# Kernel optimization log

Measured on AMD Instinct MI355X. Metric: run time of the kernel, lower is better.

Reference implementation:

```python
import jax, jax.numpy as jnp
import numpy as np

UP = 8  # nn.Upsample(scale_factor=8), nearest


def _affine_grid(theta, H, W):
    # torch F.affine_grid, align_corners=False: pixel-center normalized coords
    xs = (jnp.arange(W, dtype=jnp.float32) + 0.5) * (2.0 / W) - 1.0
    ys = (jnp.arange(H, dtype=jnp.float32) + 0.5) * (2.0 / H) - 1.0
    base = jnp.stack([
        jnp.broadcast_to(xs[None, :], (H, W)),
        jnp.broadcast_to(ys[:, None], (H, W)),
        jnp.ones((H, W), jnp.float32),
    ], axis=-1)  # [H,W,3] = (x, y, 1)
    return jnp.einsum('hwk,bjk->bhwj', base, theta)  # [B,H,W,2], last dim = (x, y)


def _grid_sample(img, grid):
    # bilinear, padding_mode='zeros', align_corners=False (torch defaults)
    B, C, H, W = img.shape
    ix = ((grid[..., 0] + 1.0) * W - 1.0) * 0.5  # [B,Ho,Wo]
    iy = ((grid[..., 1] + 1.0) * H - 1.0) * 0.5
    ix0 = jnp.floor(ix)
    iy0 = jnp.floor(iy)
    wx1 = ix - ix0
    wy1 = iy - iy0

    def corner(xc, yc, w):
        valid = (xc >= 0) & (xc <= W - 1) & (yc >= 0) & (yc <= H - 1)
        xk = jnp.clip(xc, 0, W - 1).astype(jnp.int32)
        yk = jnp.clip(yc, 0, H - 1).astype(jnp.int32)
        g = jax.vmap(lambda im, yy, xx: im[:, yy, xx])(img, yk, xk)  # [B,C,Ho,Wo]
        return g * (w * valid.astype(img.dtype))[:, None, :, :]

    return (corner(ix0, iy0, (1.0 - wx1) * (1.0 - wy1))
            + corner(ix0 + 1.0, iy0, wx1 * (1.0 - wy1))
            + corner(ix0, iy0 + 1.0, (1.0 - wx1) * wy1)
            + corner(ix0 + 1.0, iy0 + 1.0, wx1 * wy1))


def setup_inputs() -> dict:
    key = jax.random.key(0)
    k1, k2 = jax.random.split(key)
    gt = jax.random.normal(k1, (8, 1, 128, 256), dtype=jnp.float32)
    theta = jax.random.normal(k2, (8, 6), dtype=jnp.float32)
    return {"gt": gt, "theta": theta, "output_sizex": 2048, "output_sizey": 1024}


def reference(gt, theta, output_sizex, output_sizey):
    onlyy = jnp.array([0., 0., 0., 0., 1., 1.], jnp.float32)
    offset = jnp.array([1., 0., 0., 0., 0., 0.], jnp.float32)
    thetay = (theta * onlyy + offset).reshape(-1, 2, 3)  # [[1,0,0],[0,t4,t5]]
    th = theta.reshape(-1, 2, 3)
    # nearest upsample x8
    gt_up = jnp.repeat(jnp.repeat(gt, UP, axis=2), UP, axis=3)
    grid = _affine_grid(th, output_sizey, output_sizex)
    box = _grid_sample(gt_up, grid)
    gridy = _affine_grid(thetay, output_sizey, output_sizex)
    boxy = _grid_sample(gt_up, gridy)
    return (box, boxy)
```

## Files before the change

kernel.cpp:

```cpp
#include <hip/hip_runtime.h>
#include <stdint.h>


typedef float vfloat4 __attribute__((ext_vector_type(4)));

constexpr int BATCH = 8;
constexpr int HI = 128, WI = 256;
constexpr int HO = 1024, WO = 2048;
constexpr size_t NPIX = (size_t)BATCH * HO * WO;

constexpr int QH = HI + 2;
constexpr int QW = WI + 2;
constexpr size_t QIMG = (size_t)QH * QW;

__global__ __launch_bounds__(256) void pad4_kernel(
    const float* __restrict__ gt, vfloat4* __restrict__ Q)
{
    const int i = blockIdx.x * 256 + threadIdx.x;
    if (i >= (int)(BATCH * QIMG)) return;
    const int b = i / (int)QIMG;
    const int r = i - b * (int)QIMG;
    const int y = r / QW - 1;
    const int x = r - (r / QW) * QW - 1;
    const float* __restrict__ g = gt + (size_t)b * (HI * WI);
    auto val = [&](int yy, int xx) -> float {
        return (yy >= 0 && yy < HI && xx >= 0 && xx < WI)
                   ? g[yy * WI + xx] : 0.0f;
    };
    vfloat4 q = { val(y, x), val(y, x + 1), val(y + 1, x), val(y + 1, x + 1) };
    Q[i] = q;
}

__global__ __launch_bounds__(256) void stn_kernel(
    const float* __restrict__ gt,
    const float* __restrict__ theta,
    const vfloat4* __restrict__ Q,
    float* __restrict__ out)
{
    const int row = blockIdx.x;
    const int b = row >> 10;
    const int h = row & (HO - 1);
    const int t = threadIdx.x;

    const float* tb = theta + b * 6;
    const float t0 = tb[0], t1 = tb[1], t2 = tb[2];
    const float t3 = tb[3], t4 = tb[4], t5 = tb[5];
    const float* __restrict__ gtb = gt + b * (HI * WI);
    const vfloat4* __restrict__ Qb = Q + (size_t)b * QIMG + QW + 1;

    const float ys = (h + 0.5f) * (2.0f / (float)HO) - 1.0f;
    const float dix = t0;
    const float diy = 0.5f * t3;

    const float gy2 = t4 * ys + t5;
    const float iyy = ((gy2 + 1.0f) * (float)HO - 1.0f) * 0.5f;
    const float fyy = floorf(iyy);
    const float wyy = iyy - fyy;
    const float vy0 = (fyy >= 0.0f && fyy <= (float)(HO - 1)) ? 1.0f : 0.0f;
    const float vy1 = (fyy >= -1.0f && fyy <= (float)(HO - 2)) ? 1.0f : 0.0f;
    const int y0 = ((int)fminf(fmaxf(fyy,        0.0f), (float)(HO - 1))) >> 3;
    const int y1 = ((int)fminf(fmaxf(fyy + 1.0f, 0.0f), (float)(HO - 1))) >> 3;
    const float wA = (1.0f - wyy) * vy0;
    const float wB = wyy * vy1;

    float* const outrow  = out + (size_t)row * WO;
    float* const outrowy = out + NPIX + (size_t)row * WO;

#pragma unroll
    for (int s = 0; s < 2; ++s) {
        const int w0s = (s << 10) + (t << 2);

        {
            const int cell = w0s >> 3;
            const float s0 = gtb[y0 * WI + cell];
            const float s1 = gtb[y1 * WI + cell];
            const float byv = s0 * wA + s1 * wB;
            const vfloat4 vb = {byv, byv, byv, byv};
            *reinterpret_cast<vfloat4*>(outrowy + w0s) = vb;
        }

        const float xn0 = (w0s + 0.5f) * (2.0f / (float)WO) - 1.0f;
        const float gx0 = t0 * xn0 + (t1 * ys + t2);
        const float gy0 = t3 * xn0 + (t4 * ys + t5);
        const float ix0 = ((gx0 + 1.0f) * (float)WO - 1.0f) * 0.5f;
        const float iy0 = ((gy0 + 1.0f) * (float)HO - 1.0f) * 0.5f;

        const float ixe = ix0 + 3.0f * dix;
        const float iye = iy0 + 3.0f * diy;
        const float ixmin = fminf(ix0, ixe), ixmax = fmaxf(ix0, ixe);
        const float iymin = fminf(iy0, iye), iymax = fmaxf(iy0, iye);
        const bool segzero = (ixmax < -1.0f) || (ixmin >= (float)WO) ||
                             (iymax < -1.0f) || (iymin >= (float)HO);
        const bool segsafe = (ixmin >= -1.0f) && (ixmax < (float)WO) &&
                             (iymin >= -1.0f) && (iymax < (float)HO);

        float px[4];
        if (segzero) {
#pragma unroll
            for (int p = 0; p < 4; ++p) px[p] = 0.0f;
        } else if (segsafe) {
            vfloat4 q[4];
            float wx[4], wy[4];
            bool cxe[4], cye[4];
#pragma unroll
            for (int p = 0; p < 4; ++p) {
                const float ixp = fmaf((float)p, dix, ix0);
                const float iyp = fmaf((float)p, diy, iy0);
                const float fx = floorf(ixp), fy = floorf(iyp);
                wx[p] = ixp - fx;  wy[p] = iyp - fy;
                const int xi = (int)fx, yi = (int)fy;
                const int cx0 = xi >> 3;
                const int cx1 = (xi + 1) >> 3;
                const int cy0 = yi >> 3;
                const int cy1 = (yi + 1) >> 3;
                cxe[p] = (cx1 == cx0);
                cye[p] = (cy1 == cy0);
                q[p] = Qb[cy0 * QW + cx0];
            }
#pragma unroll
            for (int p = 0; p < 4; ++p) {
                const float a  = q[p].x;
                const float bb = cxe[p] ? q[p].x : q[p].y;
                const float c  = cye[p] ? q[p].x : q[p].z;
                const float dl = cxe[p] ? q[p].z : q[p].w;
                const float d  = cye[p] ? bb     : dl;
                const float h0 = fmaf(wx[p], bb - a, a);
                const float h1 = fmaf(wx[p], d - c,  c);
                px[p] = fmaf(wy[p], h1 - h0, h0);
            }
        } else {
            float ix = ix0, iy = iy0;
#pragma unroll
            for (int p = 0; p < 4; ++p) {
                const float fx = floorf(ix), fy = floorf(iy);
                const float wx = ix - fx,    wy = iy - fy;
                const int xi = (int)fx, yi = (int)fy;
                const int cx0 = min(max(xi >> 3,       -1), WI);
                const int cx1 = min(max((xi + 1) >> 3, -1), WI);
                const int cy0 = min(max(yi >> 3,       -1), HI);
                const int cy1 = min(max((yi + 1) >> 3, -1), HI);
                const vfloat4 q = Qb[cy0 * QW + cx0];
                const bool cxe = (cx1 == cx0);
                const bool cye = (cy1 == cy0);
                const float a  = q.x;
                const float bb = cxe ? q.x : q.y;
                const float c  = cye ? q.x : q.z;
                const float dl = cxe ? q.z : q.w;
                const float d  = cye ? bb  : dl;
                const float h0 = fmaf(wx, bb - a, a);
                const float h1 = fmaf(wx, d - c,  c);
                px[p] = fmaf(wy, h1 - h0, h0);
                ix += dix; iy += diy;
            }
        }
        const vfloat4 v = {px[0], px[1], px[2], px[3]};
        *reinterpret_cast<vfloat4*>(outrow + w0s) = v;
    }
}

extern "C" void kernel_launch(void* const* d_in, const int* in_sizes, int n_in,
                              void* d_out, int out_size, void* d_ws, size_t ws_size,
                              hipStream_t stream) {
    const float* gt    = (const float*)d_in[0];
    const float* theta = (const float*)d_in[1];
    float* out = (float*)d_out;
    vfloat4* Q = (vfloat4*)d_ws;

    const int qN = (int)(BATCH * QIMG);
    pad4_kernel<<<(qN + 255) / 256, 256, 0, stream>>>(gt, Q);
    stn_kernel<<<BATCH * HO, 256, 0, stream>>>(gt, theta, Q, out);
}
```

Measured before the change: 143.7 us.

## Tile output into 32x32 2D blocks and use nontemporal stores

New measurement: 147.2 us. 1.02x slower.

```diff
diff --git a/kernel.cpp b/kernel.cpp
--- a/kernel.cpp
+++ b/kernel.cpp
@@ -37,10 +37,15 @@
     const vfloat4* __restrict__ Q,
     float* __restrict__ out)
 {
-    const int row = blockIdx.x;
-    const int b = row >> 10;
-    const int h = row & (HO - 1);
-    const int t = threadIdx.x;
+    const int bid = blockIdx.x;
+    const int xt = bid & 63;
+    const int yt = (bid >> 6) & 31;
+    const int b  = bid >> 11;
+    const int tx = threadIdx.x & 7;
+    const int ty = threadIdx.x >> 3;
+    const int h  = yt * 32 + ty;
+    const int w0 = xt * 32 + tx * 4;
+    const int row = (b << 10) + h;
 
     const float* tb = theta + b * 6;
     const float t0 = tb[0], t1 = tb[1], t2 = tb[2];
@@ -52,110 +57,101 @@
     const float dix = t0;
     const float diy = 0.5f * t3;
 
-    const float gy2 = t4 * ys + t5;
-    const float iyy = ((gy2 + 1.0f) * (float)HO - 1.0f) * 0.5f;
-    const float fyy = floorf(iyy);
-    const float wyy = iyy - fyy;
-    const float vy0 = (fyy >= 0.0f && fyy <= (float)(HO - 1)) ? 1.0f : 0.0f;
-    const float vy1 = (fyy >= -1.0f && fyy <= (float)(HO - 2)) ? 1.0f : 0.0f;
-    const int y0 = ((int)fminf(fmaxf(fyy,        0.0f), (float)(HO - 1))) >> 3;
-    const int y1 = ((int)fminf(fmaxf(fyy + 1.0f, 0.0f), (float)(HO - 1))) >> 3;
-    const float wA = (1.0f - wyy) * vy0;
-    const float wB = wyy * vy1;
+    {
+        const float gy2 = t4 * ys + t5;
+        const float iyy = ((gy2 + 1.0f) * (float)HO - 1.0f) * 0.5f;
+        const float fyy = floorf(iyy);
+        const float wyy = iyy - fyy;
+        const float vy0 = (fyy >= 0.0f && fyy <= (float)(HO - 1)) ? 1.0f : 0.0f;
+        const float vy1 = (fyy >= -1.0f && fyy <= (float)(HO - 2)) ? 1.0f : 0.0f;
+        const int y0 = ((int)fminf(fmaxf(fyy,        0.0f), (float)(HO - 1))) >> 3;
+        const int y1 = ((int)fminf(fmaxf(fyy + 1.0f, 0.0f), (float)(HO - 1))) >> 3;
+        const int cell = w0 >> 3;
+        const float s0 = gtb[y0 * WI + cell];
+        const float s1 = gtb[y1 * WI + cell];
+        const float byv = s0 * ((1.0f - wyy) * vy0) + s1 * (wyy * vy1);
+        const vfloat4 vb = {byv, byv, byv, byv};
+        vfloat4* dst = reinterpret_cast<vfloat4*>(out + NPIX + (size_t)row * WO + w0);
+        __builtin_nontemporal_store(vb, dst);
+    }
 
-    float* const outrow  = out + (size_t)row * WO;
-    float* const outrowy = out + NPIX + (size_t)row * WO;
+    const float xn0 = (w0 + 0.5f) * (2.0f / (float)WO) - 1.0f;
+    const float gx0 = t0 * xn0 + (t1 * ys + t2);
+    const float gy0 = t3 * xn0 + (t4 * ys + t5);
+    const float ix0 = ((gx0 + 1.0f) * (float)WO - 1.0f) * 0.5f;
+    const float iy0 = ((gy0 + 1.0f) * (float)HO - 1.0f) * 0.5f;
 
+    const float ixe = ix0 + 3.0f * dix;
+    const float iye = iy0 + 3.0f * diy;
+    const float ixmin = fminf(ix0, ixe), ixmax = fmaxf(ix0, ixe);
+    const float iymin = fminf(iy0, iye), iymax = fmaxf(iy0, iye);
+    const bool segzero = (ixmax < -1.0f) || (ixmin >= (float)WO) ||
+                         (iymax < -1.0f) || (iymin >= (float)HO);
+    const bool segsafe = (ixmin >= -1.0f) && (ixmax < (float)WO) &&
+                         (iymin >= -1.0f) && (iymax < (float)HO);
+
+    float px[4];
+    if (segzero) {
 #pragma unroll
-    for (int s = 0; s < 2; ++s) {
-        const int w0s = (s << 10) + (t << 2);
-
-        {
-            const int cell = w0s >> 3;
-            const float s0 = gtb[y0 * WI + cell];
-            const float s1 = gtb[y1 * WI + cell];
-            const float byv = s0 * wA + s1 * wB;
-            const vfloat4 vb = {byv, byv, byv, byv};
-            *reinterpret_cast<vfloat4*>(outrowy + w0s) = vb;
+        for (int p = 0; p < 4; ++p) px[p] = 0.0f;
+    } else if (segsafe) {
+        vfloat4 q[4];
+        float wx[4], wy[4];
+        bool cxe[4], cye[4];
+#pragma unroll
+        for (int p = 0; p < 4; ++p) {
+            const float ixp = fmaf((float)p, dix, ix0);
+            const float iyp = fmaf((float)p, diy, iy0);
+            const float fx = floorf(ixp), fy = floorf(iyp);
+            wx[p] = ixp - fx;  wy[p] = iyp - fy;
+            const int xi = (int)fx, yi = (int)fy;
+            const int cx0 = xi >> 3;
+            const int cx1 = (xi + 1) >> 3;
+            const int cy0 = yi >> 3;
+            const int cy1 = (yi + 1) >> 3;
+            cxe[p] = (cx1 == cx0);
+            cye[p] = (cy1 == cy0);
+            q[p] = Qb[cy0 * QW + cx0];
         }
-
-        const float xn0 = (w0s + 0.5f) * (2.0f / (float)WO) - 1.0f;
-        const float gx0 = t0 * xn0 + (t1 * ys + t2);
-        const float gy0 = t3 * xn0 + (t4 * ys + t5);
-        const float ix0 = ((gx0 + 1.0f) * (float)WO - 1.0f) * 0.5f;
-        const float iy0 = ((gy0 + 1.0f) * (float)HO - 1.0f) * 0.5f;
-
-        const float ixe = ix0 + 3.0f * dix;
-        const float iye = iy0 + 3.0f * diy;
-        const float ixmin = fminf(ix0, ixe), ixmax = fmaxf(ix0, ixe);
-        const float iymin = fminf(iy0, iye), iymax = fmaxf(iy0, iye);
-        const bool segzero = (ixmax < -1.0f) || (ixmin >= (float)WO) ||
-                             (iymax < -1.0f) || (iymin >= (float)HO);
-        const bool segsafe = (ixmin >= -1.0f) && (ixmax < (float)WO) &&
-                             (iymin >= -1.0f) && (iymax < (float)HO);
-
-        float px[4];
-        if (segzero) {
 #pragma unroll
-            for (int p = 0; p < 4; ++p) px[p] = 0.0f;
-        } else if (segsafe) {
-            vfloat4 q[4];
-            float wx[4], wy[4];
-            bool cxe[4], cye[4];
+        for (int p = 0; p < 4; ++p) {
+            const float a  = q[p].x;
+            const float bb = cxe[p] ? q[p].x : q[p].y;
+            const float c  = cye[p] ? q[p].x : q[p].z;
+            const float dl = cxe[p] ? q[p].z : q[p].w;
+            const float d  = cye[p] ? bb     : dl;
+            const float h0 = fmaf(wx[p], bb - a, a);
+            const float h1 = fmaf(wx[p], d - c,  c);
+            px[p] = fmaf(wy[p], h1 - h0, h0);
+        }
+    } else {
+        float ix = ix0, iy = iy0;
 #pragma unroll
-            for (int p = 0; p < 4; ++p) {
-                const float ixp = fmaf((float)p, dix, ix0);
-                const float iyp = fmaf((float)p, diy, iy0);
-                const float fx = floorf(ixp), fy = floorf(iyp);
-                wx[p] = ixp - fx;  wy[p] = iyp - fy;
-                const int xi = (int)fx, yi = (int)fy;
-                const int cx0 = xi >> 3;
-                const int cx1 = (xi + 1) >> 3;
-                const int cy0 = yi >> 3;
-                const int cy1 = (yi + 1) >> 3;
-                cxe[p] = (cx1 == cx0);
-                cye[p] = (cy1 == cy0);
-                q[p] = Qb[cy0 * QW + cx0];
-            }
-#pragma unroll
-            for (int p = 0; p < 4; ++p) {
-                const float a  = q[p].x;
-                const float bb = cxe[p] ? q[p].x : q[p].y;
-                const float c  = cye[p] ? q[p].x : q[p].z;
-                const float dl = cxe[p] ? q[p].z : q[p].w;
-                const float d  = cye[p] ? bb     : dl;
-                const float h0 = fmaf(wx[p], bb - a, a);
-                const float h1 = fmaf(wx[p], d - c,  c);
-                px[p] = fmaf(wy[p], h1 - h0, h0);
-            }
-        } else {
-            float ix = ix0, iy = iy0;
-#pragma unroll
-            for (int p = 0; p < 4; ++p) {
-                const float fx = floorf(ix), fy = floorf(iy);
-                const float wx = ix - fx,    wy = iy - fy;
-                const int xi = (int)fx, yi = (int)fy;
-                const int cx0 = min(max(xi >> 3,       -1), WI);
-                const int cx1 = min(max((xi + 1) >> 3, -1), WI);
-                const int cy0 = min(max(yi >> 3,       -1), HI);
-                const int cy1 = min(max((yi + 1) >> 3, -1), HI);
-                const vfloat4 q = Qb[cy0 * QW + cx0];
-                const bool cxe = (cx1 == cx0);
-                const bool cye = (cy1 == cy0);
-                const float a  = q.x;
-                const float bb = cxe ? q.x : q.y;
-                const float c  = cye ? q.x : q.z;
-                const float dl = cxe ? q.z : q.w;
-                const float d  = cye ? bb  : dl;
-                const float h0 = fmaf(wx, bb - a, a);
-                const float h1 = fmaf(wx, d - c,  c);
-                px[p] = fmaf(wy, h1 - h0, h0);
-                ix += dix; iy += diy;
-            }
+        for (int p = 0; p < 4; ++p) {
+            const float fx = floorf(ix), fy = floorf(iy);
+            const float wx = ix - fx,    wy = iy - fy;
+            const int xi = (int)fx, yi = (int)fy;
+            const int cx0 = min(max(xi >> 3,       -1), WI);
+            const int cx1 = min(max((xi + 1) >> 3, -1), WI);
+            const int cy0 = min(max(yi >> 3,       -1), HI);
+            const int cy1 = min(max((yi + 1) >> 3, -1), HI);
+            const vfloat4 q = Qb[cy0 * QW + cx0];
+            const bool cxe = (cx1 == cx0);
+            const bool cye = (cy1 == cy0);
+            const float a  = q.x;
+            const float bb = cxe ? q.x : q.y;
+            const float c  = cye ? q.x : q.z;
+            const float dl = cxe ? q.z : q.w;
+            const float d  = cye ? bb  : dl;
+            const float h0 = fmaf(wx, bb - a, a);
+            const float h1 = fmaf(wx, d - c,  c);
+            px[p] = fmaf(wy, h1 - h0, h0);
+            ix += dix; iy += diy;
         }
-        const vfloat4 v = {px[0], px[1], px[2], px[3]};
-        *reinterpret_cast<vfloat4*>(outrow + w0s) = v;
     }
+    const vfloat4 v = {px[0], px[1], px[2], px[3]};
+    vfloat4* dst = reinterpret_cast<vfloat4*>(out + (size_t)row * WO + w0);
+    __builtin_nontemporal_store(v, dst);
 }
 
 extern "C" void kernel_launch(void* const* d_in, const int* in_sizes, int n_in,
@@ -168,5 +164,5 @@
 
     const int qN = (int)(BATCH * QIMG);
     pad4_kernel<<<(qN + 255) / 256, 256, 0, stream>>>(gt, Q);
-    stn_kernel<<<BATCH * HO, 256, 0, stream>>>(gt, theta, Q, out);
+    stn_kernel<<<BATCH * 32 * 64, 256, 0, stream>>>(gt, theta, Q, out);
 }
```
